# Performance work log

Measured on AMD Instinct MI355X. Metric: run time of the kernel, lower is better.

## Reference

```python
import jax, jax.numpy as jnp
import numpy as np


def setup_inputs() -> dict:
    key = jax.random.key(0)
    k1, k2 = jax.random.split(key)
    B, N, M, D = 8, 4096, 4096, 3
    return {
        "input": jax.random.normal(k1, (B, N, D), dtype=jnp.float32),
        "target": jax.random.normal(k2, (B, M, D), dtype=jnp.float32),
    }


def reference(input, target):
    x2 = jnp.sum(input * input, axis=-1)          # [B, N]
    y2 = jnp.sum(target * target, axis=-1)        # [B, M]
    xy = jnp.einsum("bnd,bmd->bnm", input, target)  # [B, N, M]
    sqdist = x2[:, :, None] + y2[:, None, :] - 2.0 * xy
    sqdist = jnp.maximum(sqdist, 0.0)  # clamp numerical negatives
    sqdist1 = jnp.min(sqdist, axis=2)  # nearest target for each input point [B, N]
    sqdist2 = jnp.min(sqdist, axis=1)  # nearest input for each target point [B, M]
    return jnp.mean(sqdist1) + jnp.mean(sqdist2)
```

## Files before the change

kernel.cpp:

```cpp
#include <hip/hip_runtime.h>
#include <math.h>

#define BATCH  8
#define NPTS   4096
#define TPB    256
#define QPT    8
#define QCHUNK (TPB * QPT)
#define NQC    (NPTS / QCHUNK)
#define NCC    32
#define CTILE  (NPTS / NCC)
#define NQTOT  (2 * BATCH * NPTS)

__global__ __launch_bounds__(TPB, 2) void chamfer_min_kernel(
    const float* __restrict__ input,
    const float* __restrict__ target,
    float* __restrict__ partial)
{
    const int dir = blockIdx.z;
    const int b   = blockIdx.y;
    const int qc  = blockIdx.x & (NQC - 1);
    const int cc  = blockIdx.x >> 1;

    const float* __restrict__ qp = (dir ? target : input) + (size_t)b * NPTS * 3;
    const float* __restrict__ cp = (dir ? input  : target) + (size_t)b * NPTS * 3;

    __shared__ float4 cand[CTILE];
    if (threadIdx.x < CTILE) {
        const int c = cc * CTILE + threadIdx.x;
        const float cx = cp[3 * c + 0];
        const float cy = cp[3 * c + 1];
        const float cz = cp[3 * c + 2];
        cand[threadIdx.x] = make_float4(-2.0f * cx, -2.0f * cy, -2.0f * cz,
                                        fmaf(cx, cx, fmaf(cy, cy, cz * cz)));
    }

    const int q0 = qc * QCHUNK + (int)threadIdx.x * QPT;
    float qf[3 * QPT];
    {
        const float4* qp4 = (const float4*)(qp + 3 * q0);
        #pragma unroll
        for (int j = 0; j < 6; ++j) {
            const float4 v = qp4[j];
            qf[4 * j + 0] = v.x; qf[4 * j + 1] = v.y;
            qf[4 * j + 2] = v.z; qf[4 * j + 3] = v.w;
        }
    }
    float pmin[QPT];
    #pragma unroll
    for (int k = 0; k < QPT; ++k) pmin[k] = 3.4e38f;
    __syncthreads();

    #pragma unroll 2
    for (int m = 0; m < CTILE; m += 2) {
        const float4 c0 = cand[m];
        const float4 c1 = cand[m + 1];
        #pragma unroll
        for (int k = 0; k < QPT; ++k) {
            const float d0 = fmaf(qf[3*k+0], c0.x,
                             fmaf(qf[3*k+1], c0.y,
                             fmaf(qf[3*k+2], c0.z, c0.w)));
            const float d1 = fmaf(qf[3*k+0], c1.x,
                             fmaf(qf[3*k+1], c1.y,
                             fmaf(qf[3*k+2], c1.z, c1.w)));
            pmin[k] = fminf(pmin[k], fminf(d0, d1));
        }
    }

    float res[QPT];
    #pragma unroll
    for (int k = 0; k < QPT; ++k) {
        const float x2 = fmaf(qf[3*k+0], qf[3*k+0],
                         fmaf(qf[3*k+1], qf[3*k+1],
                              qf[3*k+2] * qf[3*k+2]));
        res[k] = fmaxf(pmin[k] + x2, 0.0f);
    }
    float4* pout = (float4*)(partial + (size_t)cc * NQTOT +
                             ((size_t)(dir * BATCH + b)) * NPTS + q0);
    pout[0] = make_float4(res[0], res[1], res[2], res[3]);
    pout[1] = make_float4(res[4], res[5], res[6], res[7]);
}

__global__ __launch_bounds__(TPB) void chamfer_reduce_kernel(
    const float* __restrict__ partial, float* __restrict__ out)
{
    const int g = blockIdx.x * TPB + (int)threadIdx.x;
    float v = partial[g];
    #pragma unroll 8
    for (int cc = 1; cc < NCC; ++cc)
        v = fminf(v, partial[(size_t)cc * NQTOT + g]);

    float s = v;
    #pragma unroll
    for (int off = 32; off > 0; off >>= 1)
        s += __shfl_down(s, off, 64);

    __shared__ float wsum[TPB / 64];
    if ((threadIdx.x & 63) == 0) wsum[threadIdx.x >> 6] = s;
    __syncthreads();
    if (threadIdx.x == 0) {
        const float t = wsum[0] + wsum[1] + wsum[2] + wsum[3];
        atomicAdd(out, t * (1.0f / (float)(BATCH * NPTS)));
    }
}

extern "C" void kernel_launch(void* const* d_in, const int* in_sizes, int n_in,
                              void* d_out, int out_size, void* d_ws, size_t ws_size,
                              hipStream_t stream) {
    const float* input  = (const float*)d_in[0];
    const float* target = (const float*)d_in[1];
    float* out = (float*)d_out;
    float* partial = (float*)d_ws;

    dim3 grid1(NQC * NCC, BATCH, 2);
    chamfer_min_kernel<<<grid1, dim3(TPB), 0, stream>>>(input, target, partial);

    chamfer_reduce_kernel<<<dim3(NQTOT / TPB), dim3(TPB), 0, stream>>>(partial, out);
}
```

Measured before the change: 87.36 us.

## Precompute candidate float4s in a prep kernel and read them directly from global memory

Adds a prep kernel that converts each point into a (-2x, -2y, -2z, |c|^2) float4 in workspace. The min kernel then reads candidates straight from global memory through uniform loads instead of staging them in shared memory, which removes the LDS fill and the __syncthreads. The inner loop unroll is also raised from 2 to 4. The cost is an extra kernel launch plus a workspace round trip, and the hot loop now depends on cached global-load latency instead of LDS reads.

```diff
diff --git a/kernel.cpp b/kernel.cpp
--- a/kernel.cpp
+++ b/kernel.cpp
@@ -10,10 +10,27 @@
 #define NCC    32
 #define CTILE  (NPTS / NCC)
 #define NQTOT  (2 * BATCH * NPTS)
+#define NPREP  (2 * BATCH * NPTS)
+
+__global__ __launch_bounds__(TPB) void chamfer_prep_kernel(
+    const float* __restrict__ input, const float* __restrict__ target,
+    float4* __restrict__ prep)
+{
+    const int g   = blockIdx.x * TPB + (int)threadIdx.x;
+    const int dir = g >> 15;
+    const int p   = g & (BATCH * NPTS - 1);
+    const float* __restrict__ src = dir ? input : target;
+    const float cx = src[3 * p + 0];
+    const float cy = src[3 * p + 1];
+    const float cz = src[3 * p + 2];
+    prep[g] = make_float4(-2.0f * cx, -2.0f * cy, -2.0f * cz,
+                          fmaf(cx, cx, fmaf(cy, cy, cz * cz)));
+}
 
 __global__ __launch_bounds__(TPB, 2) void chamfer_min_kernel(
     const float* __restrict__ input,
     const float* __restrict__ target,
+    const float4* __restrict__ prep,
     float* __restrict__ partial)
 {
     const int dir = blockIdx.z;
@@ -22,17 +39,8 @@
     const int cc  = blockIdx.x >> 1;
 
     const float* __restrict__ qp = (dir ? target : input) + (size_t)b * NPTS * 3;
-    const float* __restrict__ cp = (dir ? input  : target) + (size_t)b * NPTS * 3;
-
-    __shared__ float4 cand[CTILE];
-    if (threadIdx.x < CTILE) {
-        const int c = cc * CTILE + threadIdx.x;
-        const float cx = cp[3 * c + 0];
-        const float cy = cp[3 * c + 1];
-        const float cz = cp[3 * c + 2];
-        cand[threadIdx.x] = make_float4(-2.0f * cx, -2.0f * cy, -2.0f * cz,
-                                        fmaf(cx, cx, fmaf(cy, cy, cz * cz)));
-    }
+    const float4* __restrict__ cand =
+        prep + ((size_t)dir * BATCH * NPTS + (size_t)b * NPTS + (size_t)cc * CTILE);
 
     const int q0 = qc * QCHUNK + (int)threadIdx.x * QPT;
     float qf[3 * QPT];
@@ -48,9 +56,8 @@
     float pmin[QPT];
     #pragma unroll
     for (int k = 0; k < QPT; ++k) pmin[k] = 3.4e38f;
-    __syncthreads();
 
-    #pragma unroll 2
+    #pragma unroll 4
     for (int m = 0; m < CTILE; m += 2) {
         const float4 c0 = cand[m];
         const float4 c1 = cand[m + 1];
@@ -109,10 +116,13 @@
     const float* input  = (const float*)d_in[0];
     const float* target = (const float*)d_in[1];
     float* out = (float*)d_out;
-    float* partial = (float*)d_ws;
+    float4* prep   = (float4*)d_ws;
+    float* partial = (float*)((char*)d_ws + NPREP * sizeof(float4));
+
+    chamfer_prep_kernel<<<dim3(NPREP / TPB), dim3(TPB), 0, stream>>>(input, target, prep);
 
     dim3 grid1(NQC * NCC, BATCH, 2);
-    chamfer_min_kernel<<<grid1, dim3(TPB), 0, stream>>>(input, target, partial);
+    chamfer_min_kernel<<<grid1, dim3(TPB), 0, stream>>>(input, target, prep, partial);
 
     chamfer_reduce_kernel<<<dim3(NQTOT / TPB), dim3(TPB), 0, stream>>>(partial, out);
 }
```

Result: slower. 98.31 us (+12.5%).
